# Performance work log

Measured on AMD Instinct MI355X. Metric: run time of the kernel, lower is better.

The kernel has to match this reference:

```python
import jax, jax.numpy as jnp
import numpy as np

N = 50000      # nodes
E = 800000     # edges (before self-loops)
IN_C = 128
HID = 64
HEADS = 4
OUT_C = 64
NEG_SLOPE = 0.2  # PyG GATConv default


def setup_inputs() -> dict:
    key = jax.random.key(0)
    ks = jax.random.split(key, 12)
    def glorot(k, shape, fan):
        return jax.random.normal(k, shape, jnp.float32) * (1.0 / np.sqrt(fan))
    return {
        "x": jax.random.normal(ks[0], (N, IN_C), jnp.float32),
        "edge_index": jax.random.randint(ks[1], (2, E), 0, N, dtype=jnp.int32),
        # layer 1: in -> heads*hid, concat=True
        "W1": glorot(ks[2], (IN_C, HEADS * HID), IN_C),
        "att1_src": glorot(ks[3], (HEADS, HID), HID),
        "att1_dst": glorot(ks[4], (HEADS, HID), HID),
        "b1": jnp.zeros((HEADS * HID,), jnp.float32),
        # layer 2: heads*hid -> out, heads=1
        "W2": glorot(ks[5], (HEADS * HID, OUT_C), HEADS * HID),
        "att2_src": glorot(ks[6], (1, OUT_C), OUT_C),
        "att2_dst": glorot(ks[7], (1, OUT_C), OUT_C),
        "b2": jnp.zeros((OUT_C,), jnp.float32),
    }


def gat_conv(x, src, dst, W, a_src, a_dst, b, heads):
    """One PyG-style GATConv (self-loops already included in src/dst)."""
    n = x.shape[0]
    c = W.shape[1] // heads
    h = (x @ W).reshape(n, heads, c)                    # [N,H,C]
    alpha_s = jnp.sum(h * a_src, axis=-1)               # [N,H]
    alpha_d = jnp.sum(h * a_dst, axis=-1)               # [N,H]
    e = jax.nn.leaky_relu(alpha_s[src] + alpha_d[dst], NEG_SLOPE)  # [E',H]
    # segment softmax over incoming edges of each destination node
    m = jax.ops.segment_max(e, dst, num_segments=n)
    m = jnp.where(jnp.isfinite(m), m, 0.0)
    ex = jnp.exp(e - m[dst])
    denom = jax.ops.segment_sum(ex, dst, num_segments=n)
    alpha = ex / (denom[dst] + 1e-16)                   # [E',H]
    msg = h[src] * alpha[..., None]                     # [E',H,C]
    out = jax.ops.segment_sum(msg, dst, num_segments=n) # [N,H,C]
    return out.reshape(n, heads * c) + b


def reference(x, edge_index, W1, att1_src, att1_dst, b1, W2, att2_src, att2_dst, b2):
    n = x.shape[0]
    loop = jnp.arange(n, dtype=edge_index.dtype)
    src = jnp.concatenate([edge_index[0], loop])
    dst = jnp.concatenate([edge_index[1], loop])
    # dropout is identity in eval mode
    h = gat_conv(x, src, dst, W1, att1_src, att1_dst, b1, HEADS)
    h = jax.nn.elu(h)
    return gat_conv(h, src, dst, W2, att2_src, att2_dst, b2, 1)
```

## Files before the change

### kernel.cpp

```cpp
#include <hip/hip_runtime.h>
#include <hip/hip_bf16.h>

#define NNODES 50000
#define NEDGES 800000
#define EPLUS  (NEDGES + NNODES)
#define INC    128
#define HID    64
#define NHEADS 4
#define OUTC   64
#define NEG_SLOPE 0.2f
#define STRIDE 48
#define NSLOTS (NNODES * STRIDE)

typedef __attribute__((ext_vector_type(8))) short short8;
typedef __attribute__((ext_vector_type(4))) float floatx4;

__global__ void k_uvec(const float* __restrict__ W1, const float* __restrict__ a1s,
                       const float* __restrict__ a1d, float* __restrict__ us,
                       float* __restrict__ ud) {
    int i = threadIdx.x + blockIdx.x * blockDim.x;
    if (i >= NHEADS * INC) return;
    int h = i >> 7, k = i & 127;
    const float* wp = W1 + (size_t)k * (NHEADS * HID) + h * HID;
    const float* sp = a1s + h * HID;
    const float* dp = a1d + h * HID;
    float s = 0.f, d = 0.f;
#pragma unroll 8
    for (int c = 0; c < HID; c++) { float w = wp[c]; s += w * sp[c]; d += w * dp[c]; }
    us[i] = s; ud[i] = d;
}

__global__ void k_prep_x(const float* __restrict__ x, const float* __restrict__ us,
                         const float* __restrict__ ud, __hip_bfloat16* __restrict__ xb,
                         float* __restrict__ as1, float* __restrict__ ad1) {
    int w = threadIdx.x >> 6;
    int lane = threadIdx.x & 63;
    int n = blockIdx.x * 4 + w;
    if (n >= NNODES) return;
    float2 xv = *(const float2*)(x + (size_t)n * INC + lane * 2);
    __hip_bfloat16 o[2];
    o[0] = __float2bfloat16(xv.x);
    o[1] = __float2bfloat16(xv.y);
    *(unsigned*)(xb + (size_t)n * INC + lane * 2) = *(unsigned*)o;
    float ps[4], pd[4];
#pragma unroll
    for (int h = 0; h < 4; h++) {
        float2 sv = *(const float2*)(us + h * INC + lane * 2);
        float2 dv = *(const float2*)(ud + h * INC + lane * 2);
        ps[h] = xv.x * sv.x + xv.y * sv.y;
        pd[h] = xv.x * dv.x + xv.y * dv.y;
    }
#pragma unroll
    for (int off = 1; off < 64; off <<= 1) {
#pragma unroll
        for (int h = 0; h < 4; h++) {
            ps[h] += __shfl_xor(ps[h], off, 64);
            pd[h] += __shfl_xor(pd[h], off, 64);
        }
    }
    if (lane == 0) {
        float4 vs = {ps[0], ps[1], ps[2], ps[3]};
        float4 vd = {pd[0], pd[1], pd[2], pd[3]};
        *(float4*)&as1[n * 4] = vs;
        *(float4*)&ad1[n * 4] = vd;
    }
}


__global__ void k_scat_w1(const int* __restrict__ ei, int* __restrict__ cursor,
                          const float* __restrict__ as, const float* __restrict__ ad,
                          int* __restrict__ col_src, float* __restrict__ w1e) {
    int e = blockIdx.x * blockDim.x + threadIdx.x;
    if (e >= EPLUS) return;
    int src, dst;
    if (e < NEDGES) { src = ei[e]; dst = ei[NEDGES + e]; }
    else            { src = dst = e - NEDGES; }
    int slot = atomicAdd(&cursor[dst], 1);
    if (slot >= STRIDE) return;
    int pos = dst * STRIDE + slot;
    col_src[pos] = src;
    float4 sv = *(const float4*)&as[src * 4];
    float4 dv = *(const float4*)&ad[dst * 4];
    float4 r;
    float t;
    t = sv.x + dv.x; t = (t > 0.f) ? t : NEG_SLOPE * t; r.x = __expf(t);
    t = sv.y + dv.y; t = (t > 0.f) ? t : NEG_SLOPE * t; r.y = __expf(t);
    t = sv.z + dv.z; t = (t > 0.f) ? t : NEG_SLOPE * t; r.z = __expf(t);
    t = sv.w + dv.w; t = (t > 0.f) ? t : NEG_SLOPE * t; r.w = __expf(t);
    *(float4*)&w1e[(size_t)pos * 4] = r;
}


__global__ void k_agg1n(const __hip_bfloat16* __restrict__ xb, const int* __restrict__ cnt,
                        const int* __restrict__ col_src, const float* __restrict__ w1e,
                        __hip_bfloat16* __restrict__ aggb) {
    int w = threadIdx.x >> 6;
    int lane = threadIdx.x & 63;
    int n = blockIdx.x * 4 + w;
    if (n >= NNODES) return;
    int deg = cnt[n]; if (deg > STRIDE) deg = STRIDE;
    int beg = n * STRIDE, end = beg + deg;
    const unsigned* xp = (const unsigned*)xb + lane;

    float accL[4] = {0.f, 0.f, 0.f, 0.f};
    float accH[4] = {0.f, 0.f, 0.f, 0.f};
    float den[4]  = {0.f, 0.f, 0.f, 0.f};

    int j = beg;
    for (; j + 3 < end; j += 4) {
        int s0 = col_src[j], s1 = col_src[j + 1], s2 = col_src[j + 2], s3 = col_src[j + 3];
        float4 w0 = *(const float4*)&w1e[(size_t)j * 4];
        float4 w1 = *(const float4*)&w1e[(size_t)(j + 1) * 4];
        float4 w2 = *(const float4*)&w1e[(size_t)(j + 2) * 4];
        float4 w3 = *(const float4*)&w1e[(size_t)(j + 3) * 4];
        unsigned u0 = xp[(size_t)s0 * 64];
        unsigned u1 = xp[(size_t)s1 * 64];
        unsigned u2 = xp[(size_t)s2 * 64];
        unsigned u3 = xp[(size_t)s3 * 64];
        float lo0 = __uint_as_float(u0 << 16), hi0 = __uint_as_float(u0 & 0xffff0000u);
        float lo1 = __uint_as_float(u1 << 16), hi1 = __uint_as_float(u1 & 0xffff0000u);
        float lo2 = __uint_as_float(u2 << 16), hi2 = __uint_as_float(u2 & 0xffff0000u);
        float lo3 = __uint_as_float(u3 << 16), hi3 = __uint_as_float(u3 & 0xffff0000u);
        accL[0] += w0.x * lo0 + w1.x * lo1 + w2.x * lo2 + w3.x * lo3;
        accH[0] += w0.x * hi0 + w1.x * hi1 + w2.x * hi2 + w3.x * hi3;
        den[0]  += (w0.x + w1.x) + (w2.x + w3.x);
        accL[1] += w0.y * lo0 + w1.y * lo1 + w2.y * lo2 + w3.y * lo3;
        accH[1] += w0.y * hi0 + w1.y * hi1 + w2.y * hi2 + w3.y * hi3;
        den[1]  += (w0.y + w1.y) + (w2.y + w3.y);
        accL[2] += w0.z * lo0 + w1.z * lo1 + w2.z * lo2 + w3.z * lo3;
        accH[2] += w0.z * hi0 + w1.z * hi1 + w2.z * hi2 + w3.z * hi3;
        den[2]  += (w0.z + w1.z) + (w2.z + w3.z);
        accL[3] += w0.w * lo0 + w1.w * lo1 + w2.w * lo2 + w3.w * lo3;
        accH[3] += w0.w * hi0 + w1.w * hi1 + w2.w * hi2 + w3.w * hi3;
        den[3]  += (w0.w + w1.w) + (w2.w + w3.w);
    }
    for (; j < end; j++) {
        int s0 = col_src[j];
        float4 w0 = *(const float4*)&w1e[(size_t)j * 4];
        unsigned u0 = xp[(size_t)s0 * 64];
        float lo = __uint_as_float(u0 << 16), hi = __uint_as_float(u0 & 0xffff0000u);
        accL[0] += w0.x * lo; accH[0] += w0.x * hi; den[0] += w0.x;
        accL[1] += w0.y * lo; accH[1] += w0.y * hi; den[1] += w0.y;
        accL[2] += w0.z * lo; accH[2] += w0.z * hi; den[2] += w0.z;
        accL[3] += w0.w * lo; accH[3] += w0.w * hi; den[3] += w0.w;
    }
#pragma unroll
    for (int h = 0; h < 4; h++) {
        float inv = 1.f / (den[h] + 1e-16f);
        __hip_bfloat16 o[2];
        o[0] = __float2bfloat16(accL[h] * inv);
        o[1] = __float2bfloat16(accH[h] * inv);
        *(unsigned*)(aggb + ((size_t)n * NHEADS + h) * INC + lane * 2) = *(unsigned*)o;
    }
}


__global__ void k_swz1(const float* __restrict__ W1, __hip_bfloat16* __restrict__ Bsw) {
    int i = blockIdx.x * blockDim.x + threadIdx.x;
    if (i >= 4 * 4 * 4 * 64 * 8) return;
    int j = i & 7, l = (i >> 3) & 63, t = (i >> 9) & 3, s = (i >> 11) & 3, h = i >> 13;
    int k = s * 32 + (l >> 4) * 8 + j;
    int col = h * 64 + t * 16 + (l & 15);
    Bsw[i] = __float2bfloat16(W1[(size_t)k * 256 + col]);
}

__global__ void k_swz2(const float* __restrict__ W2, __hip_bfloat16* __restrict__ Bsw) {
    int i = blockIdx.x * blockDim.x + threadIdx.x;
    if (i >= 8 * 4 * 64 * 8) return;
    int j = i & 7, l = (i >> 3) & 63, t = (i >> 9) & 3, s = i >> 11;
    int k = s * 32 + (l >> 4) * 8 + j;
    int col = t * 16 + (l & 15);
    Bsw[i] = __float2bfloat16(W2[(size_t)k * 64 + col]);
}


__global__ void k_mm1(const __hip_bfloat16* __restrict__ A,
                      const __hip_bfloat16* __restrict__ Bsw,
                      const float* __restrict__ b1,
                      __hip_bfloat16* __restrict__ out1b) {
    int row0 = blockIdx.x * 64;
    int h = blockIdx.y;
    int w = threadIdx.x >> 6;
    int l = threadIdx.x & 63;
    int lg = l >> 4, lm = l & 15;
    int ra = row0 + w * 16 + lm;
    if (ra >= NNODES) ra = NNODES - 1;

    floatx4 acc[4];
#pragma unroll
    for (int t = 0; t < 4; t++) acc[t] = (floatx4){0.f, 0.f, 0.f, 0.f};

    const __hip_bfloat16* ap = A + ((size_t)ra * NHEADS + h) * INC + lg * 8;
#pragma unroll
    for (int s = 0; s < 4; s++) {
        short8 a = *(const short8*)(ap + s * 32);
#pragma unroll
        for (int t = 0; t < 4; t++) {
            short8 b = *(const short8*)(Bsw + (((h * 4 + s) * 4 + t) * 64 + l) * 8);
            acc[t] = __builtin_amdgcn_mfma_f32_16x16x32_bf16(a, b, acc[t], 0, 0, 0);
        }
    }
#pragma unroll
    for (int t = 0; t < 4; t++) {
        int col = h * 64 + t * 16 + lm;
        float bias = b1[col];
#pragma unroll
        for (int r = 0; r < 4; r++) {
            int row = row0 + w * 16 + lg * 4 + r;
            if (row < NNODES) {
                float v = acc[t][r] + bias;
                v = (v > 0.f) ? v : (__expf(v) - 1.f);
                out1b[(size_t)row * 256 + col] = __float2bfloat16(v);
            }
        }
    }
}


__global__ void k_mm2(const __hip_bfloat16* __restrict__ A,
                      const __hip_bfloat16* __restrict__ Bsw,
                      const float* __restrict__ a2s, const float* __restrict__ a2d,
                      __hip_bfloat16* __restrict__ h2b,
                      float* __restrict__ as2, float* __restrict__ ad2) {
    int row0 = blockIdx.x * 64;
    int w = threadIdx.x >> 6;
    int l = threadIdx.x & 63;
    int lg = l >> 4, lm = l & 15;
    int ra = row0 + w * 16 + lm;
    if (ra >= NNODES) ra = NNODES - 1;

    floatx4 acc[4];
#pragma unroll
    for (int t = 0; t < 4; t++) acc[t] = (floatx4){0.f, 0.f, 0.f, 0.f};

    const __hip_bfloat16* ap = A + (size_t)ra * 256 + lg * 8;
#pragma unroll
    for (int s = 0; s < 8; s++) {
        short8 a = *(const short8*)(ap + s * 32);
#pragma unroll
        for (int t = 0; t < 4; t++) {
            short8 b = *(const short8*)(Bsw + ((s * 4 + t) * 64 + l) * 8);
            acc[t] = __builtin_amdgcn_mfma_f32_16x16x32_bf16(a, b, acc[t], 0, 0, 0);
        }
    }
    float ps[4] = {0.f, 0.f, 0.f, 0.f};
    float pd[4] = {0.f, 0.f, 0.f, 0.f};
#pragma unroll
    for (int t = 0; t < 4; t++) {
        int col = t * 16 + lm;
        float vs = a2s[col], vd = a2d[col];
#pragma unroll
        for (int r = 0; r < 4; r++) {
            int row = row0 + w * 16 + lg * 4 + r;
            float v = acc[t][r];
            if (row < NNODES) h2b[(size_t)row * OUTC + col] = __float2bfloat16(v);
            ps[r] += v * vs;
            pd[r] += v * vd;
        }
    }
#pragma unroll
    for (int off = 1; off < 16; off <<= 1) {
#pragma unroll
        for (int r = 0; r < 4; r++) {
            ps[r] += __shfl_xor(ps[r], off, 64);
            pd[r] += __shfl_xor(pd[r], off, 64);
        }
    }
    if (lm == 0) {
#pragma unroll
        for (int r = 0; r < 4; r++) {
            int row = row0 + w * 16 + lg * 4 + r;
            if (row < NNODES) { as2[row] = ps[r]; ad2[row] = pd[r]; }
        }
    }
}


__global__ void k_edgew2(const int* __restrict__ col_src, const int* __restrict__ cnt,
                         const float* __restrict__ as, const float* __restrict__ ad,
                         float* __restrict__ w) {
    int e = blockIdx.x * blockDim.x + threadIdx.x;
    if (e >= NSLOTS) return;
    int n = e / STRIDE;
    int slot = e - n * STRIDE;
    int deg = cnt[n]; if (deg > STRIDE) deg = STRIDE;
    if (slot >= deg) return;
    float t = as[col_src[e]] + ad[n];
    t = (t > 0.f) ? t : NEG_SLOPE * t;
    w[e] = __expf(t);
}


__global__ void k_agg2n(const __hip_bfloat16* __restrict__ h2b, const int* __restrict__ cnt,
                        const int* __restrict__ col_src, const float* __restrict__ w2e,
                        const float* __restrict__ b2, float* __restrict__ out) {
    int w = threadIdx.x >> 6;
    int lane = threadIdx.x & 63;
    int n = blockIdx.x * 4 + w;
    if (n >= NNODES) return;
    int deg = cnt[n]; if (deg > STRIDE) deg = STRIDE;
    int beg = n * STRIDE, end = beg + deg;
    const __hip_bfloat16* hp = h2b + lane;

    float acc = 0.f, den = 0.f;
    int j = beg;
    for (; j + 3 < end; j += 4) {
        int s0 = col_src[j], s1 = col_src[j + 1], s2 = col_src[j + 2], s3 = col_src[j + 3];
        float w0 = w2e[j], w1 = w2e[j + 1], w2 = w2e[j + 2], w3 = w2e[j + 3];
        float g0 = __bfloat162float(hp[(size_t)s0 * OUTC]);
        float g1 = __bfloat162float(hp[(size_t)s1 * OUTC]);
        float g2 = __bfloat162float(hp[(size_t)s2 * OUTC]);
        float g3 = __bfloat162float(hp[(size_t)s3 * OUTC]);
        acc += w0 * g0 + w1 * g1 + w2 * g2 + w3 * g3;
        den += (w0 + w1) + (w2 + w3);
    }
    for (; j < end; j++) {
        int s0 = col_src[j];
        float w0 = w2e[j];
        acc += w0 * __bfloat162float(hp[(size_t)s0 * OUTC]);
        den += w0;
    }
    out[(size_t)n * OUTC + lane] = acc / (den + 1e-16f) + b2[lane];
}


extern "C" void kernel_launch(void* const* d_in, const int* in_sizes, int n_in,
                              void* d_out, int out_size, void* d_ws, size_t ws_size,
                              hipStream_t stream) {
    const float* x   = (const float*)d_in[0];
    const int*   ei  = (const int*)d_in[1];
    const float* W1  = (const float*)d_in[2];
    const float* a1s = (const float*)d_in[3];
    const float* a1d = (const float*)d_in[4];
    const float* b1  = (const float*)d_in[5];
    const float* W2  = (const float*)d_in[6];
    const float* a2s = (const float*)d_in[7];
    const float* a2d = (const float*)d_in[8];
    const float* b2  = (const float*)d_in[9];
    float* out = (float*)d_out;

    char* p = (char*)d_ws;
    auto carve = [&](size_t bytes) -> void* {
        void* r = (void*)p;
        p += (bytes + 255) & ~(size_t)255;
        return r;
    };
    __hip_bfloat16* xb    = (__hip_bfloat16*)carve((size_t)NNODES * INC * 2);
    __hip_bfloat16* aggb  = (__hip_bfloat16*)carve((size_t)NNODES * NHEADS * INC * 2);
    __hip_bfloat16* out1b = (__hip_bfloat16*)carve((size_t)NNODES * 256 * 2);
    __hip_bfloat16* h2b   = (__hip_bfloat16*)carve((size_t)NNODES * OUTC * 2);
    __hip_bfloat16* Bsw1  = (__hip_bfloat16*)carve((size_t)4 * 4 * 4 * 64 * 8 * 2);
    __hip_bfloat16* Bsw2  = (__hip_bfloat16*)carve((size_t)8 * 4 * 64 * 8 * 2);
    float* us      = (float*)carve((size_t)NHEADS * INC * 4);
    float* ud      = (float*)carve((size_t)NHEADS * INC * 4);
    float* as1     = (float*)carve((size_t)NNODES * NHEADS * 4);
    float* ad1     = (float*)carve((size_t)NNODES * NHEADS * 4);
    float* as2     = (float*)carve((size_t)NNODES * 4);
    float* ad2     = (float*)carve((size_t)NNODES * 4);
    int*   cursor  = (int*)carve((size_t)NNODES * 4);
    int*   col_src = (int*)carve((size_t)NSLOTS * 4);
    float* w1e     = (float*)carve((size_t)NSLOTS * 4 * 4);
    float* w2e     = (float*)carve((size_t)NSLOTS * 4);

    hipMemsetAsync(cursor, 0, (size_t)NNODES * 4, stream);
    k_uvec<<<2, 256, 0, stream>>>(W1, a1s, a1d, us, ud);
    k_prep_x<<<(NNODES + 3) / 4, 256, 0, stream>>>(x, us, ud, xb, as1, ad1);
    k_swz1<<<(4 * 4 * 4 * 64 * 8 + 255) / 256, 256, 0, stream>>>(W1, Bsw1);
    k_swz2<<<(8 * 4 * 64 * 8 + 255) / 256, 256, 0, stream>>>(W2, Bsw2);

    k_scat_w1<<<(EPLUS + 255) / 256, 256, 0, stream>>>(ei, cursor, as1, ad1, col_src, w1e);

    k_agg1n<<<(NNODES + 3) / 4, 256, 0, stream>>>(xb, cursor, col_src, w1e, aggb);
    dim3 g1((NNODES + 63) / 64, NHEADS);
    k_mm1<<<g1, 256, 0, stream>>>(aggb, Bsw1, b1, out1b);

    k_mm2<<<(NNODES + 63) / 64, 256, 0, stream>>>(out1b, Bsw2, a2s, a2d, h2b, as2, ad2);
    k_edgew2<<<(NSLOTS + 255) / 256, 256, 0, stream>>>(col_src, cursor, as2, ad2, w2e);
    k_agg2n<<<(NNODES + 3) / 4, 256, 0, stream>>>(h2b, cursor, col_src, w2e, b2, out);
}
```

Before: 302.0 us.

## Pack edge src and fp16 weights into int4 records; fuse layer-2 edge weights into aggregation

Layer-1 edge data now goes into one 16-byte record per slot: the source index plus four attention exp-weights stored as fp16. Before, it was a separate int index array and a float4 weight array, so each edge now needs one vector load instead of two. The k_edgew2 kernel is removed, and layer 2 computes its exp-weights inline in k_agg2n by gathering as2[src]. This cuts a launch and a full pass over the slot array. In exchange it adds fp16 precision loss on the layer-1 weights, a possible fp16 overflow if a logit exceeds about 11, and a 4-byte gather per edge in layer 2.

```diff
diff --git a/kernel.cpp b/kernel.cpp
--- a/kernel.cpp
+++ b/kernel.cpp
@@ -1,5 +1,6 @@
 #include <hip/hip_runtime.h>
 #include <hip/hip_bf16.h>
+#include <hip/hip_fp16.h>
 
 #define NNODES 50000
 #define NEDGES 800000
@@ -69,7 +70,7 @@
 
 __global__ void k_scat_w1(const int* __restrict__ ei, int* __restrict__ cursor,
                           const float* __restrict__ as, const float* __restrict__ ad,
-                          int* __restrict__ col_src, float* __restrict__ w1e) {
+                          int4* __restrict__ rec) {
     int e = blockIdx.x * blockDim.x + threadIdx.x;
     if (e >= EPLUS) return;
     int src, dst;
@@ -78,22 +79,26 @@
     int slot = atomicAdd(&cursor[dst], 1);
     if (slot >= STRIDE) return;
     int pos = dst * STRIDE + slot;
-    col_src[pos] = src;
     float4 sv = *(const float4*)&as[src * 4];
     float4 dv = *(const float4*)&ad[dst * 4];
-    float4 r;
-    float t;
-    t = sv.x + dv.x; t = (t > 0.f) ? t : NEG_SLOPE * t; r.x = __expf(t);
-    t = sv.y + dv.y; t = (t > 0.f) ? t : NEG_SLOPE * t; r.y = __expf(t);
-    t = sv.z + dv.z; t = (t > 0.f) ? t : NEG_SLOPE * t; r.z = __expf(t);
-    t = sv.w + dv.w; t = (t > 0.f) ? t : NEG_SLOPE * t; r.w = __expf(t);
-    *(float4*)&w1e[(size_t)pos * 4] = r;
+    float t, w0, w1, w2, w3;
+    t = sv.x + dv.x; t = (t > 0.f) ? t : NEG_SLOPE * t; w0 = __expf(t);
+    t = sv.y + dv.y; t = (t > 0.f) ? t : NEG_SLOPE * t; w1 = __expf(t);
+    t = sv.z + dv.z; t = (t > 0.f) ? t : NEG_SLOPE * t; w2 = __expf(t);
+    t = sv.w + dv.w; t = (t > 0.f) ? t : NEG_SLOPE * t; w3 = __expf(t);
+    __half2 p01 = __floats2half2_rn(w0, w1);
+    __half2 p23 = __floats2half2_rn(w2, w3);
+    int4 rc;
+    rc.x = src;
+    rc.y = *(int*)&p01;
+    rc.z = *(int*)&p23;
+    rc.w = 0;
+    rec[pos] = rc;
 }
 
 
 __global__ void k_agg1n(const __hip_bfloat16* __restrict__ xb, const int* __restrict__ cnt,
-                        const int* __restrict__ col_src, const float* __restrict__ w1e,
-                        __hip_bfloat16* __restrict__ aggb) {
+                        const int4* __restrict__ rec, __hip_bfloat16* __restrict__ aggb) {
     int w = threadIdx.x >> 6;
     int lane = threadIdx.x & 63;
     int n = blockIdx.x * 4 + w;
@@ -108,41 +113,44 @@
 
     int j = beg;
     for (; j + 3 < end; j += 4) {
-        int s0 = col_src[j], s1 = col_src[j + 1], s2 = col_src[j + 2], s3 = col_src[j + 3];
-        float4 w0 = *(const float4*)&w1e[(size_t)j * 4];
-        float4 w1 = *(const float4*)&w1e[(size_t)(j + 1) * 4];
-        float4 w2 = *(const float4*)&w1e[(size_t)(j + 2) * 4];
-        float4 w3 = *(const float4*)&w1e[(size_t)(j + 3) * 4];
-        unsigned u0 = xp[(size_t)s0 * 64];
-        unsigned u1 = xp[(size_t)s1 * 64];
-        unsigned u2 = xp[(size_t)s2 * 64];
-        unsigned u3 = xp[(size_t)s3 * 64];
-        float lo0 = __uint_as_float(u0 << 16), hi0 = __uint_as_float(u0 & 0xffff0000u);
-        float lo1 = __uint_as_float(u1 << 16), hi1 = __uint_as_float(u1 & 0xffff0000u);
-        float lo2 = __uint_as_float(u2 << 16), hi2 = __uint_as_float(u2 & 0xffff0000u);
-        float lo3 = __uint_as_float(u3 << 16), hi3 = __uint_as_float(u3 & 0xffff0000u);
-        accL[0] += w0.x * lo0 + w1.x * lo1 + w2.x * lo2 + w3.x * lo3;
-        accH[0] += w0.x * hi0 + w1.x * hi1 + w2.x * hi2 + w3.x * hi3;
-        den[0]  += (w0.x + w1.x) + (w2.x + w3.x);
-        accL[1] += w0.y * lo0 + w1.y * lo1 + w2.y * lo2 + w3.y * lo3;
-        accH[1] += w0.y * hi0 + w1.y * hi1 + w2.y * hi2 + w3.y * hi3;
-        den[1]  += (w0.y + w1.y) + (w2.y + w3.y);
-        accL[2] += w0.z * lo0 + w1.z * lo1 + w2.z * lo2 + w3.z * lo3;
-        accH[2] += w0.z * hi0 + w1.z * hi1 + w2.z * hi2 + w3.z * hi3;
-        den[2]  += (w0.z + w1.z) + (w2.z + w3.z);
-        accL[3] += w0.w * lo0 + w1.w * lo1 + w2.w * lo2 + w3.w * lo3;
-        accH[3] += w0.w * hi0 + w1.w * hi1 + w2.w * hi2 + w3.w * hi3;
-        den[3]  += (w0.w + w1.w) + (w2.w + w3.w);
+        int4 r0 = rec[j], r1 = rec[j + 1], r2 = rec[j + 2], r3 = rec[j + 3];
+        unsigned u0 = xp[(size_t)r0.x * 64];
+        unsigned u1 = xp[(size_t)r1.x * 64];
+        unsigned u2 = xp[(size_t)r2.x * 64];
+        unsigned u3 = xp[(size_t)r3.x * 64];
+        int4 rr[4] = {r0, r1, r2, r3};
+        unsigned uu[4] = {u0, u1, u2, u3};
+#pragma unroll
+        for (int q = 0; q < 4; q++) {
+            __half2 p01 = *(__half2*)&rr[q].y;
+            __half2 p23 = *(__half2*)&rr[q].z;
+            float wt[4] = {__low2float(p01), __high2float(p01),
+                           __low2float(p23), __high2float(p23)};
+            float lo = __uint_as_float(uu[q] << 16);
+            float hi = __uint_as_float(uu[q] & 0xffff0000u);
+#pragma unroll
+            for (int h = 0; h < 4; h++) {
+                accL[h] += wt[h] * lo;
+                accH[h] += wt[h] * hi;
+                den[h]  += wt[h];
+            }
+        }
     }
     for (; j < end; j++) {
-        int s0 = col_src[j];
-        float4 w0 = *(const float4*)&w1e[(size_t)j * 4];
-        unsigned u0 = xp[(size_t)s0 * 64];
-        float lo = __uint_as_float(u0 << 16), hi = __uint_as_float(u0 & 0xffff0000u);
-        accL[0] += w0.x * lo; accH[0] += w0.x * hi; den[0] += w0.x;
-        accL[1] += w0.y * lo; accH[1] += w0.y * hi; den[1] += w0.y;
-        accL[2] += w0.z * lo; accH[2] += w0.z * hi; den[2] += w0.z;
-        accL[3] += w0.w * lo; accH[3] += w0.w * hi; den[3] += w0.w;
+        int4 r0 = rec[j];
+        unsigned u0 = xp[(size_t)r0.x * 64];
+        __half2 p01 = *(__half2*)&r0.y;
+        __half2 p23 = *(__half2*)&r0.z;
+        float wt[4] = {__low2float(p01), __high2float(p01),
+                       __low2float(p23), __high2float(p23)};
+        float lo = __uint_as_float(u0 << 16);
+        float hi = __uint_as_float(u0 & 0xffff0000u);
+#pragma unroll
+        for (int h = 0; h < 4; h++) {
+            accL[h] += wt[h] * lo;
+            accH[h] += wt[h] * hi;
+            den[h]  += wt[h];
+        }
     }
 #pragma unroll
     for (int h = 0; h < 4; h++) {
@@ -276,47 +284,41 @@
 }
 
 
-__global__ void k_edgew2(const int* __restrict__ col_src, const int* __restrict__ cnt,
-                         const float* __restrict__ as, const float* __restrict__ ad,
-                         float* __restrict__ w) {
-    int e = blockIdx.x * blockDim.x + threadIdx.x;
-    if (e >= NSLOTS) return;
-    int n = e / STRIDE;
-    int slot = e - n * STRIDE;
-    int deg = cnt[n]; if (deg > STRIDE) deg = STRIDE;
-    if (slot >= deg) return;
-    float t = as[col_src[e]] + ad[n];
-    t = (t > 0.f) ? t : NEG_SLOPE * t;
-    w[e] = __expf(t);
-}
-
-
 __global__ void k_agg2n(const __hip_bfloat16* __restrict__ h2b, const int* __restrict__ cnt,
-                        const int* __restrict__ col_src, const float* __restrict__ w2e,
-                        const float* __restrict__ b2, float* __restrict__ out) {
+                        const int4* __restrict__ rec, const float* __restrict__ as2,
+                        const float* __restrict__ ad2, const float* __restrict__ b2,
+                        float* __restrict__ out) {
     int w = threadIdx.x >> 6;
     int lane = threadIdx.x & 63;
     int n = blockIdx.x * 4 + w;
     if (n >= NNODES) return;
     int deg = cnt[n]; if (deg > STRIDE) deg = STRIDE;
     int beg = n * STRIDE, end = beg + deg;
+    float adv = ad2[n];
     const __hip_bfloat16* hp = h2b + lane;
 
     float acc = 0.f, den = 0.f;
     int j = beg;
     for (; j + 3 < end; j += 4) {
-        int s0 = col_src[j], s1 = col_src[j + 1], s2 = col_src[j + 2], s3 = col_src[j + 3];
-        float w0 = w2e[j], w1 = w2e[j + 1], w2 = w2e[j + 2], w3 = w2e[j + 3];
+        int s0 = rec[j].x, s1 = rec[j + 1].x, s2 = rec[j + 2].x, s3 = rec[j + 3].x;
+        float t0 = as2[s0] + adv, t1 = as2[s1] + adv;
+        float t2 = as2[s2] + adv, t3 = as2[s3] + adv;
         float g0 = __bfloat162float(hp[(size_t)s0 * OUTC]);
         float g1 = __bfloat162float(hp[(size_t)s1 * OUTC]);
         float g2 = __bfloat162float(hp[(size_t)s2 * OUTC]);
         float g3 = __bfloat162float(hp[(size_t)s3 * OUTC]);
+        t0 = (t0 > 0.f) ? t0 : NEG_SLOPE * t0; float w0 = __expf(t0);
+        t1 = (t1 > 0.f) ? t1 : NEG_SLOPE * t1; float w1 = __expf(t1);
+        t2 = (t2 > 0.f) ? t2 : NEG_SLOPE * t2; float w2 = __expf(t2);
+        t3 = (t3 > 0.f) ? t3 : NEG_SLOPE * t3; float w3 = __expf(t3);
         acc += w0 * g0 + w1 * g1 + w2 * g2 + w3 * g3;
         den += (w0 + w1) + (w2 + w3);
     }
     for (; j < end; j++) {
-        int s0 = col_src[j];
-        float w0 = w2e[j];
+        int s0 = rec[j].x;
+        float t0 = as2[s0] + adv;
+        t0 = (t0 > 0.f) ? t0 : NEG_SLOPE * t0;
+        float w0 = __expf(t0);
         acc += w0 * __bfloat162float(hp[(size_t)s0 * OUTC]);
         den += w0;
     }
@@ -358,9 +360,7 @@
     float* as2     = (float*)carve((size_t)NNODES * 4);
     float* ad2     = (float*)carve((size_t)NNODES * 4);
     int*   cursor  = (int*)carve((size_t)NNODES * 4);
-    int*   col_src = (int*)carve((size_t)NSLOTS * 4);
-    float* w1e     = (float*)carve((size_t)NSLOTS * 4 * 4);
-    float* w2e     = (float*)carve((size_t)NSLOTS * 4);
+    int4*  rec     = (int4*)carve((size_t)NSLOTS * 16);
 
     hipMemsetAsync(cursor, 0, (size_t)NNODES * 4, stream);
     k_uvec<<<2, 256, 0, stream>>>(W1, a1s, a1d, us, ud);
@@ -368,13 +368,12 @@
     k_swz1<<<(4 * 4 * 4 * 64 * 8 + 255) / 256, 256, 0, stream>>>(W1, Bsw1);
     k_swz2<<<(8 * 4 * 64 * 8 + 255) / 256, 256, 0, stream>>>(W2, Bsw2);
 
-    k_scat_w1<<<(EPLUS + 255) / 256, 256, 0, stream>>>(ei, cursor, as1, ad1, col_src, w1e);
-
-    k_agg1n<<<(NNODES + 3) / 4, 256, 0, stream>>>(xb, cursor, col_src, w1e, aggb);
+    k_scat_w1<<<(EPLUS + 255) / 256, 256, 0, stream>>>(ei, cursor, as1, ad1, rec);
+
+    k_agg1n<<<(NNODES + 3) / 4, 256, 0, stream>>>(xb, cursor, rec, aggb);
     dim3 g1((NNODES + 63) / 64, NHEADS);
     k_mm1<<<g1, 256, 0, stream>>>(aggb, Bsw1, b1, out1b);
 
     k_mm2<<<(NNODES + 63) / 64, 256, 0, stream>>>(out1b, Bsw2, a2s, a2d, h2b, as2, ad2);
-    k_edgew2<<<(NSLOTS + 255) / 256, 256, 0, stream>>>(col_src, cursor, as2, ad2, w2e);
-    k_agg2n<<<(NNODES + 3) / 4, 256, 0, stream>>>(h2b, cursor, col_src, w2e, b2, out);
-}
+    k_agg2n<<<(NNODES + 3) / 4, 256, 0, stream>>>(h2b, cursor, rec, as2, ad2, b2, out);
+}
```

Result: faster. 283.2 us (-6.2%).
